# Kernel optimization log

Hardware: AMD Instinct MI355X
Metric: run time of the kernel (lower is better)

## Reference

```python
import jax, jax.numpy as jnp
import numpy as np

K = 3  # number of nearest neighbors
EPS = 1e-10


def setup_inputs() -> dict:
    key = jax.random.key(0)
    k1, k2, k3 = jax.random.split(key, 3)
    B, C, N = 2, 3, 8192
    xyz1 = jax.random.normal(k1, (B, C, N), dtype=jnp.float32)
    xyz2 = jax.random.normal(k2, (B, C, N), dtype=jnp.float32)
    flow1 = jax.random.normal(k3, (B, C, N), dtype=jnp.float32) * 0.1
    return {"xyz1": xyz1, "xyz2": xyz2, "flow1": flow1}


def _square_distance(src, dst):
    # src: [B, N, 3], dst: [B, M, 3] -> [B, N, M]
    d = -2.0 * jnp.einsum('bnc,bmc->bnm', src, dst)
    d = d + jnp.sum(src ** 2, axis=-1)[:, :, None]
    d = d + jnp.sum(dst ** 2, axis=-1)[:, None, :]
    return d


def _gather_group(points, idx):
    # points: [B, N, C], idx: [B, S, K] -> [B, S, K, C]
    return jax.vmap(lambda p, i: p[i])(points, idx)


def reference(xyz1, xyz2, flow1):
    B, C, N1 = xyz1.shape
    N2 = xyz2.shape[2]
    xyz1_to_2 = (xyz1 + flow1).transpose(0, 2, 1)  # [B, N1, 3]
    xyz2_t = xyz2.transpose(0, 2, 1)               # [B, N2, 3]
    flow1_t = flow1.transpose(0, 2, 1)             # [B, N1, 3]

    sqrdists = _square_distance(xyz2_t, xyz1_to_2)  # [B, N2, N1]
    _, knn_idx = jax.lax.top_k(-sqrdists, K)        # smallest K -> [B, N2, K]

    grouped_xyz = _gather_group(xyz1_to_2, knn_idx)           # [B, N2, K, 3]
    diff = grouped_xyz - xyz2_t[:, :, None, :]                 # [B, N2, K, 3]
    dist = jnp.maximum(jnp.linalg.norm(diff, axis=3), EPS)     # [B, N2, K]
    inv = 1.0 / dist
    weight = inv / jnp.sum(inv, axis=2, keepdims=True)         # [B, N2, K]

    grouped_flow = _gather_group(flow1_t, knn_idx)             # [B, N2, K, 3]
    flow2 = jnp.sum(weight[..., None] * grouped_flow, axis=2)  # [B, N2, 3]
    warped_xyz2 = (xyz2_t - flow2).transpose(0, 2, 1)          # [B, 3, N2]
    return warped_xyz2
```

## Files before the change

### kernel.cpp

```cpp
#include <hip/hip_runtime.h>


#define NPTS   8192
#define BLOCK  256
#define Q      4
#define QPB    8
#define HALF   4096
#define KMASK  0xFFFFFF80
#define EPSV   1e-10f

__device__ __forceinline__ float rfl_f32(float x) {
    return __int_as_float(__builtin_amdgcn_readfirstlane(__float_as_int(x)));
}

__device__ __forceinline__ void insert3_idx(float k, int idx,
                                            float& m0, float& m1, float& m2,
                                            int& j0, int& j1, int& j2) {
    const bool c0 = k < m0;
    const bool c1 = k < m1;
    const bool c2 = k < m2;
    m2 = __builtin_amdgcn_fmed3f(k, m1, m2);
    m1 = __builtin_amdgcn_fmed3f(k, m0, m1);
    m0 = fminf(k, m0);
    j2 = c1 ? j1 : (c2 ? idx : j2);
    j1 = c0 ? j0 : (c1 ? idx : j1);
    j0 = c0 ? idx : j0;
}

__global__ __launch_bounds__(256)
void warp_points_kernel(const float* __restrict__ xyz1,
                        const float* __restrict__ flow1,
                        float4* __restrict__ ws, int total) {
    const int i = blockIdx.x * 256 + threadIdx.x;
    if (i >= total) return;
    const int b = i / NPTS, n = i - b * NPTS;
    const float* x1 = xyz1 + (size_t)b * 3 * NPTS;
    const float* f1 = flow1 + (size_t)b * 3 * NPTS;
    const float px = x1[0*NPTS + n] + f1[0*NPTS + n];
    const float py = x1[1*NPTS + n] + f1[1*NPTS + n];
    const float pz = x1[2*NPTS + n] + f1[2*NPTS + n];
    ws[i] = make_float4(px, py, pz, 0.0f);
}

__global__ __launch_bounds__(BLOCK, 8)
void pointwarp_kernel(const float4* __restrict__ wsp,
                      const float* __restrict__ xyz2,
                      const float* __restrict__ flow1,
                      float* __restrict__ out) {
    __shared__ float s_k[2][2][Q][3];
    __shared__ int   s_i[2][2][Q][3];

    const int tid  = threadIdx.x;
    const int w    = tid >> 6;
    const int t    = tid & 63;
    const int pair = w >> 1;
    const int w2   = w & 1;
    const int blocksPerB = NPTS / QPB;
    const int b     = blockIdx.x / blocksPerB;
    const int qblk  = (blockIdx.x % blocksPerB) * QPB;
    const int qbase = qblk + pair * Q;

    const float4* cand = wsp + (size_t)b * NPTS;
    const float*  x2   = xyz2 + (size_t)b * 3 * NPTS;
    const float*  f1   = flow1 + (size_t)b * 3 * NPTS;

    float qx[Q], qy[Q], qz[Q], k0[Q], k1[Q], k2[Q];
    #pragma unroll
    for (int i = 0; i < Q; ++i) {
        qx[i] = rfl_f32(x2[0*NPTS + qbase + i]);
        qy[i] = rfl_f32(x2[1*NPTS + qbase + i]);
        qz[i] = rfl_f32(x2[2*NPTS + qbase + i]);
        k0[i] = k1[i] = k2[i] = 3e38f;
    }

    const float4* base = cand + w2 * HALF + t;
    const int rowbase = w2 * (HALF / 64);
    #pragma unroll 4
    for (int j = 0; j < HALF / 64; ++j) {
        const float4 p = base[j * 64];
        const int jg = rowbase + j;
        #pragma unroll
        for (int i = 0; i < Q; ++i) {
            const float dx = p.x - qx[i];
            const float dy = p.y - qy[i];
            const float dz = p.z - qz[i];
            const float d  = fmaf(dx, dx, fmaf(dy, dy, dz*dz));
            const float k  = __int_as_float((__float_as_int(d) & KMASK) | jg);
            k2[i] = __builtin_amdgcn_fmed3f(k, k1[i], k2[i]);
            k1[i] = __builtin_amdgcn_fmed3f(k, k0[i], k1[i]);
            k0[i] = fminf(k, k0[i]);
        }
    }

    int i0[Q], i1[Q], i2[Q];
    #pragma unroll
    for (int i = 0; i < Q; ++i) {
        i0[i] = ((__float_as_int(k0[i]) & 0x7F) << 6) | t;
        i1[i] = ((__float_as_int(k1[i]) & 0x7F) << 6) | t;
        i2[i] = ((__float_as_int(k2[i]) & 0x7F) << 6) | t;
    }

    #pragma unroll
    for (int step = 1; step < 64; step <<= 1) {
        #pragma unroll
        for (int i = 0; i < Q; ++i) {
            const float b0 = __shfl_xor(k0[i], step, 64);
            const float b1 = __shfl_xor(k1[i], step, 64);
            const float b2 = __shfl_xor(k2[i], step, 64);
            const int   a0 = __shfl_xor(i0[i], step, 64);
            const int   a1 = __shfl_xor(i1[i], step, 64);
            const int   a2 = __shfl_xor(i2[i], step, 64);
            insert3_idx(b0, a0, k0[i], k1[i], k2[i], i0[i], i1[i], i2[i]);
            insert3_idx(b1, a1, k0[i], k1[i], k2[i], i0[i], i1[i], i2[i]);
            insert3_idx(b2, a2, k0[i], k1[i], k2[i], i0[i], i1[i], i2[i]);
        }
    }

    #pragma unroll
    for (int i = 0; i < Q; ++i) {
        if (t == i) {
            s_k[pair][w2][i][0] = k0[i]; s_i[pair][w2][i][0] = i0[i];
            s_k[pair][w2][i][1] = k1[i]; s_i[pair][w2][i][1] = i1[i];
            s_k[pair][w2][i][2] = k2[i]; s_i[pair][w2][i][2] = i2[i];
        }
    }
    __syncthreads();

    if (tid < QPB) {
        const int u  = tid;
        const int pr = u >> 2, qi = u & 3;
        float m0 = 3e38f, m1 = 3e38f, m2 = 3e38f;
        int   j0 = 0, j1 = 0, j2 = 0;
        #pragma unroll
        for (int wv = 0; wv < 2; ++wv) {
            #pragma unroll
            for (int s = 0; s < 3; ++s) {
                insert3_idx(s_k[pr][wv][qi][s], s_i[pr][wv][qi][s],
                            m0, m1, m2, j0, j1, j2);
            }
        }
        const int n2 = qblk + u;
        const float gx = x2[0*NPTS + n2];
        const float gy = x2[1*NPTS + n2];
        const float gz = x2[2*NPTS + n2];
        float dd[3];
        const int js[3] = {j0, j1, j2};
        #pragma unroll
        for (int s = 0; s < 3; ++s) {
            const float4 p = cand[js[s]];
            const float dx = p.x - gx, dy = p.y - gy, dz = p.z - gz;
            dd[s] = fmaf(dx, dx, fmaf(dy, dy, dz*dz));
        }
        float w0 = 1.0f / fmaxf(sqrtf(dd[0]), EPSV);
        float w1 = 1.0f / fmaxf(sqrtf(dd[1]), EPSV);
        float w2v = 1.0f / fmaxf(sqrtf(dd[2]), EPSV);
        const float ws = w0 + w1 + w2v;
        w0 /= ws; w1 /= ws; w2v /= ws;

        float* o = out + (size_t)b * 3 * NPTS;
        #pragma unroll
        for (int c = 0; c < 3; ++c) {
            const float fl = w0  * f1[c*NPTS + j0]
                           + w1  * f1[c*NPTS + j1]
                           + w2v * f1[c*NPTS + j2];
            o[c*NPTS + n2] = x2[c*NPTS + n2] - fl;
        }
    }
}

extern "C" void kernel_launch(void* const* d_in, const int* in_sizes, int n_in,
                              void* d_out, int out_size, void* d_ws, size_t ws_size,
                              hipStream_t stream) {
    const float* xyz1  = (const float*)d_in[0];
    const float* xyz2  = (const float*)d_in[1];
    const float* flow1 = (const float*)d_in[2];
    float* out = (float*)d_out;
    float4* ws = (float4*)d_ws;

    const int B = in_sizes[0] / (3 * NPTS);
    const int total = B * NPTS;
    warp_points_kernel<<<(total + 255) / 256, 256, 0, stream>>>(xyz1, flow1, ws, total);
    const int grid = B * (NPTS / QPB);
    pointwarp_kernel<<<grid, BLOCK, 0, stream>>>(ws, xyz2, flow1, out);
}
```

Before: 104.2 us.

## Drop index shuffles in wave top-3 reduction; recover lanes via ballot

The butterfly reduction now shuffles only the packed distance keys and no longer carries the three lane indices with them, which cuts the shuffle count per step in half and removes the index select logic. After the reduction, each wave finds the lane that owns each winning key with a ballot on exact key equality and takes the first set bit. The candidate scan loop is also restructured to load two points per iteration with unroll 2. If two lanes hold bit-identical keys, the first lane wins, which may change tie behaviour compared with the old per-lane index tracking.

Result: faster. 97.96 us (-6.0%).

```diff
diff --git a/kernel.cpp b/kernel.cpp
--- a/kernel.cpp
+++ b/kernel.cpp
@@ -13,15 +13,19 @@
     return __int_as_float(__builtin_amdgcn_readfirstlane(__float_as_int(x)));
 }
 
+__device__ __forceinline__ void ksort3(float k, float& m0, float& m1, float& m2) {
+    m2 = __builtin_amdgcn_fmed3f(k, m1, m2);
+    m1 = __builtin_amdgcn_fmed3f(k, m0, m1);
+    m0 = fminf(k, m0);
+}
+
 __device__ __forceinline__ void insert3_idx(float k, int idx,
                                             float& m0, float& m1, float& m2,
                                             int& j0, int& j1, int& j2) {
     const bool c0 = k < m0;
     const bool c1 = k < m1;
     const bool c2 = k < m2;
-    m2 = __builtin_amdgcn_fmed3f(k, m1, m2);
-    m1 = __builtin_amdgcn_fmed3f(k, m0, m1);
-    m0 = fminf(k, m0);
+    ksort3(k, m0, m1, m2);
     j2 = c1 ? j1 : (c2 ? idx : j2);
     j1 = c0 ? j0 : (c1 ? idx : j1);
     j0 = c0 ? idx : j0;
@@ -75,30 +79,32 @@
 
     const float4* base = cand + w2 * HALF + t;
     const int rowbase = w2 * (HALF / 64);
-    #pragma unroll 4
-    for (int j = 0; j < HALF / 64; ++j) {
-        const float4 p = base[j * 64];
-        const int jg = rowbase + j;
+    #pragma unroll 2
+    for (int j = 0; j < HALF / 128; ++j) {
+        const float4 p0 = base[j * 128];
+        const float4 p1 = base[j * 128 + 64];
+        const int jg0 = rowbase + 2*j;
+        const int jg1 = jg0 + 1;
         #pragma unroll
         for (int i = 0; i < Q; ++i) {
-            const float dx = p.x - qx[i];
-            const float dy = p.y - qy[i];
-            const float dz = p.z - qz[i];
-            const float d  = fmaf(dx, dx, fmaf(dy, dy, dz*dz));
-            const float k  = __int_as_float((__float_as_int(d) & KMASK) | jg);
-            k2[i] = __builtin_amdgcn_fmed3f(k, k1[i], k2[i]);
-            k1[i] = __builtin_amdgcn_fmed3f(k, k0[i], k1[i]);
-            k0[i] = fminf(k, k0[i]);
-        }
-    }
-
-    int i0[Q], i1[Q], i2[Q];
-    #pragma unroll
-    for (int i = 0; i < Q; ++i) {
-        i0[i] = ((__float_as_int(k0[i]) & 0x7F) << 6) | t;
-        i1[i] = ((__float_as_int(k1[i]) & 0x7F) << 6) | t;
-        i2[i] = ((__float_as_int(k2[i]) & 0x7F) << 6) | t;
-    }
+            const float dx0 = p0.x - qx[i];
+            const float dy0 = p0.y - qy[i];
+            const float dz0 = p0.z - qz[i];
+            const float d0  = fmaf(dx0, dx0, fmaf(dy0, dy0, dz0*dz0));
+            const float ka  = __int_as_float((__float_as_int(d0) & KMASK) | jg0);
+            ksort3(ka, k0[i], k1[i], k2[i]);
+            const float dx1 = p1.x - qx[i];
+            const float dy1 = p1.y - qy[i];
+            const float dz1 = p1.z - qz[i];
+            const float d1  = fmaf(dx1, dx1, fmaf(dy1, dy1, dz1*dz1));
+            const float kb  = __int_as_float((__float_as_int(d1) & KMASK) | jg1);
+            ksort3(kb, k0[i], k1[i], k2[i]);
+        }
+    }
+
+    float a0[Q], a1[Q], a2[Q];
+    #pragma unroll
+    for (int i = 0; i < Q; ++i) { a0[i] = k0[i]; a1[i] = k1[i]; a2[i] = k2[i]; }
 
     #pragma unroll
     for (int step = 1; step < 64; step <<= 1) {
@@ -107,12 +113,29 @@
             const float b0 = __shfl_xor(k0[i], step, 64);
             const float b1 = __shfl_xor(k1[i], step, 64);
             const float b2 = __shfl_xor(k2[i], step, 64);
-            const int   a0 = __shfl_xor(i0[i], step, 64);
-            const int   a1 = __shfl_xor(i1[i], step, 64);
-            const int   a2 = __shfl_xor(i2[i], step, 64);
-            insert3_idx(b0, a0, k0[i], k1[i], k2[i], i0[i], i1[i], i2[i]);
-            insert3_idx(b1, a1, k0[i], k1[i], k2[i], i0[i], i1[i], i2[i]);
-            insert3_idx(b2, a2, k0[i], k1[i], k2[i], i0[i], i1[i], i2[i]);
+            ksort3(b0, k0[i], k1[i], k2[i]);
+            ksort3(b1, k0[i], k1[i], k2[i]);
+            ksort3(b2, k0[i], k1[i], k2[i]);
+        }
+    }
+
+    int i0[Q], i1[Q], i2[Q];
+    #pragma unroll
+    for (int i = 0; i < Q; ++i) {
+        {
+            const float kf = k0[i];
+            const unsigned long long m = __ballot(kf == a0[i] || kf == a1[i] || kf == a2[i]);
+            i0[i] = ((__float_as_int(kf) & 0x7F) << 6) | (__ffsll(m) - 1);
+        }
+        {
+            const float kf = k1[i];
+            const unsigned long long m = __ballot(kf == a0[i] || kf == a1[i] || kf == a2[i]);
+            i1[i] = ((__float_as_int(kf) & 0x7F) << 6) | (__ffsll(m) - 1);
+        }
+        {
+            const float kf = k2[i];
+            const unsigned long long m = __ballot(kf == a0[i] || kf == a1[i] || kf == a2[i]);
+            i2[i] = ((__float_as_int(kf) & 0x7F) << 6) | (__ffsll(m) - 1);
         }
     }
 
```
